# Kernel optimization log

Hardware: AMD Instinct MI355X
Metric: run time of the kernel (lower is better)

The kernel has to match this reference:

```python
import jax, jax.numpy as jnp
import numpy as np

def setup_inputs() -> dict:
    key = jax.random.key(0)
    k0, k1, k2, k3 = jax.random.split(key, 4)
    B, L, D, E, Dg = 2, 2048, 2048, 8, 256  # Dg = D // E
    x = jax.random.normal(k0, (B, L, D), dtype=jnp.float32)
    Wg = jax.random.normal(k1, (E, D), dtype=jnp.float32) * 0.02     # gate: Linear(D, E)
    Wd = jax.random.normal(k2, (E, Dg, D), dtype=jnp.float32) * 0.02  # down: Linear(D, Dg) per expert
    Wu = jax.random.normal(k3, (E, D, Dg), dtype=jnp.float32) * 0.02  # up:   Linear(Dg, D) per expert
    return {"x": x, "Wg": Wg, "Wd": Wd, "Wu": Wu, "k": 2}

def reference(x, Wg, Wd, Wu, k):
    B, L, D = x.shape
    E = Wg.shape[0]
    T = B * L
    xf = x.reshape(T, D)
    # gate scores: sigmoid(x @ Wg^T), then top-k gate values G and expert indices I
    S = jax.nn.sigmoid(xf @ Wg.T)            # [T, E]
    G, I = jax.lax.top_k(S, k)               # [T, k], [T, k]
    # combine weights per token per expert (zero for unselected experts);
    # equivalent to the original's one_hot + per-expert gather/scatter-add.
    w = jnp.zeros((T, E), x.dtype).at[jnp.arange(T)[:, None], I].add(G)  # [T, E]
    # down: sum_e w[t,e] * (Wd[e] @ x[t])
    down = jnp.einsum('te,egd,td->tg', w, Wd, xf)   # [T, Dg]
    # inner model is identity
    # up: sum_e w[t,e] * (Wu[e] @ down[t])
    up = jnp.einsum('te,edg,tg->td', w, Wu, down)   # [T, D]
    return up.reshape(B, L, D)
```

## Files before the change

kernel.cpp:

```cpp
#include <hip/hip_runtime.h>
#include <stdint.h>

#define T_TOK 4096
#define DIM   2048
#define NEXP  8
#define DG    256
#define TOPK  2

#define BM 64
#define BN 128
#define BKU 64
#define NROWS  (T_TOK*TOPK + NEXP*BM)
#define NBLK_M (NROWS/BM)

typedef __attribute__((ext_vector_type(8))) short short8;
typedef __attribute__((ext_vector_type(4))) float f32x4;

static __device__ __forceinline__ short f2bf(float f) {
    union { float f; uint32_t u; } v{f};
    uint32_t r = v.u + 0x7fffu + ((v.u >> 16) & 1u);
    return (short)(r >> 16);
}
static __device__ __forceinline__ float b2f(short s) {
    union { uint32_t u; float f; } v{((uint32_t)(unsigned short)s) << 16};
    return v.f;
}

#define GLD16(g, l) \
    __builtin_amdgcn_global_load_lds((const __attribute__((address_space(1))) void*)(g), \
                                     (__attribute__((address_space(3))) void*)(l), 16, 0, 0)

__global__ __launch_bounds__(256) void gate_kernel(const float* __restrict__ x,
                                                   const float* __restrict__ Wg,
                                                   int* __restrict__ gidx,
                                                   float* __restrict__ gval,
                                                   short* __restrict__ x_bf)
{
    int token = blockIdx.x * 4 + (threadIdx.x >> 6);
    int lane  = threadIdx.x & 63;
    const float4* xr = (const float4*)(x + (size_t)token * DIM);

    float4 xv[8];
#pragma unroll
    for (int i = 0; i < 8; i++) xv[i] = xr[lane + 64 * i];

    short4* xb = (short4*)(x_bf + (size_t)token * DIM);
#pragma unroll
    for (int i = 0; i < 8; i++) {
        short4 o;
        o.x = f2bf(xv[i].x); o.y = f2bf(xv[i].y);
        o.z = f2bf(xv[i].z); o.w = f2bf(xv[i].w);
        xb[lane + 64 * i] = o;
    }

    float acc[NEXP];
#pragma unroll
    for (int e = 0; e < NEXP; e++) {
        const float4* wr = (const float4*)(Wg + e * DIM);
        float a = 0.0f;
#pragma unroll
        for (int i = 0; i < 8; i++) {
            float4 w = wr[lane + 64 * i];
            a += xv[i].x * w.x + xv[i].y * w.y + xv[i].z * w.z + xv[i].w * w.w;
        }
        acc[e] = a;
    }

#pragma unroll
    for (int m = 1; m < 64; m <<= 1) {
#pragma unroll
        for (int e = 0; e < NEXP; e++) acc[e] += __shfl_xor(acc[e], m, 64);
    }

    if (lane == 0) {
        float sg[NEXP];
#pragma unroll
        for (int e = 0; e < NEXP; e++) sg[e] = 1.0f / (1.0f + expf(-acc[e]));
        int i0 = 0;
#pragma unroll
        for (int e = 1; e < NEXP; e++) if (sg[e] > sg[i0]) i0 = e;
        int i1 = (i0 == 0) ? 1 : 0;
#pragma unroll
        for (int e = 0; e < NEXP; e++) if (e != i0 && e != i1 && sg[e] > sg[i1]) i1 = e;
        gidx[2 * token + 0] = i0;
        gidx[2 * token + 1] = i1;
        gval[2 * token + 0] = sg[i0];
        gval[2 * token + 1] = sg[i1];
    }
}

__global__ __launch_bounds__(256) void convW_kernel(const float* __restrict__ Wd,
                                                    const float* __restrict__ Wu,
                                                    short* __restrict__ Wd_bf,
                                                    short* __restrict__ Wu_bf,
                                                    int n4)
{
    int i = blockIdx.x * 256 + threadIdx.x;
    const float* s; short* d; int j;
    if (i < n4)      { s = Wd; d = Wd_bf; j = i; }
    else             { s = Wu; d = Wu_bf; j = i - n4; if (j >= n4) return; }
    float4 v = ((const float4*)s)[j];
    short4 o;
    o.x = f2bf(v.x); o.y = f2bf(v.y); o.z = f2bf(v.z); o.w = f2bf(v.w);
    ((short4*)d)[j] = o;
}

__global__ __launch_bounds__(1024) void bucket_kernel(const int* __restrict__ gidx,
                                                      int* __restrict__ rowtok,
                                                      int* __restrict__ rowpos,
                                                      int* __restrict__ seg_off)
{
    __shared__ int cnt[NEXP];
    __shared__ int cur[NEXP];
    int tid = threadIdx.x, lane = tid & 63;
    if (tid < NEXP) cnt[tid] = 0;
    __syncthreads();

    int e_[8];
#pragma unroll
    for (int r = 0; r < 8; r++) e_[r] = gidx[r * 1024 + tid];

    int mycnt = 0;
#pragma unroll
    for (int r = 0; r < 8; r++) {
        int e = e_[r];
#pragma unroll
        for (int ee = 0; ee < NEXP; ee++) {
            unsigned long long m = __ballot(e == ee);
            if (lane == ee) mycnt += (int)__popcll(m);
        }
    }
    if (lane < NEXP) atomicAdd(&cnt[lane], mycnt);
    __syncthreads();

    if (tid == 0) {
        int o = 0;
        for (int e = 0; e < NEXP; e++) {
            seg_off[e] = o;
            cur[e] = o;
            o += ((cnt[e] + BM - 1) / BM) * BM;
        }
        seg_off[NEXP] = o;
    }
    __syncthreads();

    for (int r = tid; r < NROWS; r += 1024) rowtok[r] = -1;
    __syncthreads();

#pragma unroll
    for (int r = 0; r < 8; r++) {
        int idx = r * 1024 + tid;
        int e = e_[r];
#pragma unroll
        for (int ee = 0; ee < NEXP; ee++) {
            unsigned long long m = __ballot(e == ee);
            if (m == 0) continue;
            int leader = __ffsll((unsigned long long)m) - 1;
            int base = 0;
            if (lane == leader) base = atomicAdd(&cur[ee], (int)__popcll(m));
            base = __shfl(base, leader, 64);
            if (e == ee) {
                int pos = base + (int)__popcll(m & ((1ull << lane) - 1ull));
                rowtok[pos] = idx >> 1;
                rowpos[idx] = pos;
            }
        }
    }
}

#define AS3 __attribute__((address_space(3)))

#define VMCNT(N) asm volatile("s_waitcnt vmcnt(" #N ")" ::: "memory")
#define BAR()    __builtin_amdgcn_s_barrier()

#define STAGE(B_) do { \
    GLD16(agA0, lA_##B_##_0); \
    GLD16(agA1, lA_##B_##_1); \
    GLD16(agB0, lB_##B_##_0); \
    GLD16(agB1, lB_##B_##_1); \
    GLD16(agB2, lB_##B_##_2); \
    GLD16(agB3, lB_##B_##_3); \
    agA0 += BKU; agA1 += BKU; \
    agB0 += BKU; agB1 += BKU; agB2 += BKU; agB3 += BKU; \
} while (0)

#define COMP(B_) do { \
    short8 a00 = *(const short8*)&As[B_][am0][c0]; \
    short8 a10 = *(const short8*)&As[B_][am1][c0]; \
    short8 b00 = *(const short8*)&Bs[B_][bn0][c0]; \
    short8 b10 = *(const short8*)&Bs[B_][bn1][c0]; \
    short8 b20 = *(const short8*)&Bs[B_][bn2][c0]; \
    short8 b30 = *(const short8*)&Bs[B_][bn3][c0]; \
    short8 a01 = *(const short8*)&As[B_][am0][c1]; \
    short8 a11 = *(const short8*)&As[B_][am1][c1]; \
    short8 b01 = *(const short8*)&Bs[B_][bn0][c1]; \
    short8 b11 = *(const short8*)&Bs[B_][bn1][c1]; \
    short8 b21 = *(const short8*)&Bs[B_][bn2][c1]; \
    short8 b31 = *(const short8*)&Bs[B_][bn3][c1]; \
    acc[0][0] = __builtin_amdgcn_mfma_f32_16x16x32_bf16(a00, b00, acc[0][0], 0, 0, 0); \
    acc[0][1] = __builtin_amdgcn_mfma_f32_16x16x32_bf16(a00, b10, acc[0][1], 0, 0, 0); \
    acc[0][2] = __builtin_amdgcn_mfma_f32_16x16x32_bf16(a00, b20, acc[0][2], 0, 0, 0); \
    acc[0][3] = __builtin_amdgcn_mfma_f32_16x16x32_bf16(a00, b30, acc[0][3], 0, 0, 0); \
    acc[1][0] = __builtin_amdgcn_mfma_f32_16x16x32_bf16(a10, b00, acc[1][0], 0, 0, 0); \
    acc[1][1] = __builtin_amdgcn_mfma_f32_16x16x32_bf16(a10, b10, acc[1][1], 0, 0, 0); \
    acc[1][2] = __builtin_amdgcn_mfma_f32_16x16x32_bf16(a10, b20, acc[1][2], 0, 0, 0); \
    acc[1][3] = __builtin_amdgcn_mfma_f32_16x16x32_bf16(a10, b30, acc[1][3], 0, 0, 0); \
    acc[0][0] = __builtin_amdgcn_mfma_f32_16x16x32_bf16(a01, b01, acc[0][0], 0, 0, 0); \
    acc[0][1] = __builtin_amdgcn_mfma_f32_16x16x32_bf16(a01, b11, acc[0][1], 0, 0, 0); \
    acc[0][2] = __builtin_amdgcn_mfma_f32_16x16x32_bf16(a01, b21, acc[0][2], 0, 0, 0); \
    acc[0][3] = __builtin_amdgcn_mfma_f32_16x16x32_bf16(a01, b31, acc[0][3], 0, 0, 0); \
    acc[1][0] = __builtin_amdgcn_mfma_f32_16x16x32_bf16(a11, b01, acc[1][0], 0, 0, 0); \
    acc[1][1] = __builtin_amdgcn_mfma_f32_16x16x32_bf16(a11, b11, acc[1][1], 0, 0, 0); \
    acc[1][2] = __builtin_amdgcn_mfma_f32_16x16x32_bf16(a11, b21, acc[1][2], 0, 0, 0); \
    acc[1][3] = __builtin_amdgcn_mfma_f32_16x16x32_bf16(a11, b31, acc[1][3], 0, 0, 0); \
} while (0)

template<int K, int Ntot>
__global__ __launch_bounds__(256) void gemm_kernel(const short* __restrict__ A,
                                                   const short* __restrict__ B,
                                                   const int* __restrict__ rowtok,
                                                   const int* __restrict__ seg_off,
                                                   short* __restrict__ C)
{
    __shared__ __align__(16) short As[2][BM][BKU];
    __shared__ __align__(16) short Bs[2][BN][BKU];

    int row0 = blockIdx.x * BM;
    int total = seg_off[NEXP];
    if (row0 >= total) return;
    int e = 0;
    while (row0 >= seg_off[e + 1]) ++e;
    int n0 = blockIdx.y * BN;

    int tid = threadIdx.x;
    int w = tid >> 6, l = tid & 63;

    int srow = (w << 3) + (l >> 3);
    int sc   = ((l & 7) ^ ((l >> 3) & 7)) << 3;

    int ta0 = rowtok[row0 + srow];      if (ta0 < 0) ta0 = 0;
    int ta1 = rowtok[row0 + 32 + srow]; if (ta1 < 0) ta1 = 0;
    const short* agA0 = A + (size_t)ta0 * K + sc;
    const short* agA1 = A + (size_t)ta1 * K + sc;
    const short* be = B + (size_t)e * Ntot * K + (size_t)n0 * K;
    const short* agB0 = be + (size_t)(srow     ) * K + sc;
    const short* agB1 = be + (size_t)(srow + 32) * K + sc;
    const short* agB2 = be + (size_t)(srow + 64) * K + sc;
    const short* agB3 = be + (size_t)(srow + 96) * K + sc;

    auto lA_0_0 = (AS3 void*)&As[0][(w << 3)     ][0];
    auto lA_0_1 = (AS3 void*)&As[0][(w << 3) + 32][0];
    auto lA_1_0 = (AS3 void*)&As[1][(w << 3)     ][0];
    auto lA_1_1 = (AS3 void*)&As[1][(w << 3) + 32][0];
    auto lB_0_0 = (AS3 void*)&Bs[0][(w << 3)     ][0];
    auto lB_0_1 = (AS3 void*)&Bs[0][(w << 3) + 32][0];
    auto lB_0_2 = (AS3 void*)&Bs[0][(w << 3) + 64][0];
    auto lB_0_3 = (AS3 void*)&Bs[0][(w << 3) + 96][0];
    auto lB_1_0 = (AS3 void*)&Bs[1][(w << 3)     ][0];
    auto lB_1_1 = (AS3 void*)&Bs[1][(w << 3) + 32][0];
    auto lB_1_2 = (AS3 void*)&Bs[1][(w << 3) + 64][0];
    auto lB_1_3 = (AS3 void*)&Bs[1][(w << 3) + 96][0];

    int mlane = l & 15, qlane = l >> 4;
    int wm = w >> 1, wn = w & 1;
    int c0 = (qlane ^ (mlane & 7)) << 3;
    int c1 = c0 ^ 32;
    int am0 = wm * 32 + mlane, am1 = am0 + 16;
    int bn0 = wn * 64 + mlane, bn1 = bn0 + 16, bn2 = bn0 + 32, bn3 = bn0 + 48;

    f32x4 acc[2][4] = {};

    constexpr int NT = K / BKU;
    STAGE(0);
    STAGE(1);
#pragma unroll 1
    for (int t = 0; t < NT - 2; t += 2) {
        VMCNT(6); BAR();
        COMP(0);
        BAR();
        STAGE(0);
        VMCNT(6); BAR();
        COMP(1);
        BAR();
        if (t + 3 < NT) STAGE(1);
    }
    VMCNT(6); BAR();
    COMP(0);
    BAR();
    VMCNT(0); BAR();
    COMP(1);

#pragma unroll
    for (int i = 0; i < 2; i++) {
        int rbase = row0 + wm * 32 + i * 16 + qlane * 4;
#pragma unroll
        for (int j = 0; j < 4; j++) {
            int col = n0 + wn * 64 + j * 16 + mlane;
#pragma unroll
            for (int r = 0; r < 4; r++)
                C[(size_t)(rbase + r) * Ntot + col] = f2bf(acc[i][j][r]);
        }
    }
}

#undef STAGE
#undef COMP
#undef AS3

__global__ __launch_bounds__(256) void combine1_kernel(const short* __restrict__ dr,
                                                       const int* __restrict__ rowpos,
                                                       const float* __restrict__ gval,
                                                       short* __restrict__ dt)
{
    int t = blockIdx.x, d = threadIdx.x;
    int   p0 = rowpos[2 * t], p1 = rowpos[2 * t + 1];
    float g0 = gval[2 * t],   g1 = gval[2 * t + 1];
    float v = g0 * b2f(dr[(size_t)p0 * DG + d]) + g1 * b2f(dr[(size_t)p1 * DG + d]);
    dt[(size_t)t * DG + d] = f2bf(v);
}

__global__ __launch_bounds__(256) void combine2_kernel(const short* __restrict__ ur,
                                                       const int* __restrict__ rowpos,
                                                       const float* __restrict__ gval,
                                                       float* __restrict__ out)
{
    int i = blockIdx.x * 256 + threadIdx.x;
    int t = i >> 9;
    int c = (i & 511) * 4;
    int   p0 = rowpos[2 * t], p1 = rowpos[2 * t + 1];
    float g0 = gval[2 * t],   g1 = gval[2 * t + 1];
    short4 u0 = *(const short4*)&ur[(size_t)p0 * DIM + c];
    short4 u1 = *(const short4*)&ur[(size_t)p1 * DIM + c];
    float4 o;
    o.x = g0 * b2f(u0.x) + g1 * b2f(u1.x);
    o.y = g0 * b2f(u0.y) + g1 * b2f(u1.y);
    o.z = g0 * b2f(u0.z) + g1 * b2f(u1.z);
    o.w = g0 * b2f(u0.w) + g1 * b2f(u1.w);
    *(float4*)&out[(size_t)t * DIM + c] = o;
}

extern "C" void kernel_launch(void* const* d_in, const int* in_sizes, int n_in,
                              void* d_out, int out_size, void* d_ws, size_t ws_size,
                              hipStream_t stream) {
    const float* x  = (const float*)d_in[0];
    const float* Wg = (const float*)d_in[1];
    const float* Wd = (const float*)d_in[2];
    const float* Wu = (const float*)d_in[3];
    float* out = (float*)d_out;

    char* p = (char*)d_ws;
    int*   gidx    = (int*)(p + 0);
    float* gval    = (float*)(p + 32768);
    int*   rowtok  = (int*)(p + 65536);
    int*   rowpos  = (int*)(p + 100352);
    int*   seg_off = (int*)(p + 133120);
    short* x_bf    = (short*)(p + 133376);
    short* Wd_bf   = (short*)(p + 133376 + 16777216);
    short* Wu_bf   = Wd_bf + 4194304;
    short* dr_bf   = Wu_bf + 4194304;
    short* dt_bf   = dr_bf + (size_t)NROWS * DG;
    short* ur_bf   = dt_bf + (size_t)T_TOK * DG;

    const int W4 = NEXP * DG * DIM / 4;
    gate_kernel<<<T_TOK / 4, 256, 0, stream>>>(x, Wg, gidx, gval, x_bf);
    convW_kernel<<<(2 * W4 + 255) / 256, 256, 0, stream>>>(Wd, Wu, Wd_bf, Wu_bf, W4);
    bucket_kernel<<<1, 1024, 0, stream>>>(gidx, rowtok, rowpos, seg_off);

    gemm_kernel<DIM, DG><<<dim3(NBLK_M, DG / BN), 256, 0, stream>>>(x_bf, Wd_bf, rowtok, seg_off, dr_bf);
    combine1_kernel<<<T_TOK, 256, 0, stream>>>(dr_bf, rowpos, gval, dt_bf);
    gemm_kernel<DG, DIM><<<dim3(NBLK_M, DIM / BN), 256, 0, stream>>>(dt_bf, Wu_bf, rowtok, seg_off, ur_bf);
    combine2_kernel<<<T_TOK * DIM / 4 / 256, 256, 0, stream>>>(ur_bf, rowpos, gval, out);
}
```

Before: 204.9 us.

## Fuse gate with weight conversion, fold combine1 into up-GEMM, remap blocks for XCDs

```diff
diff --git a/kernel.cpp b/kernel.cpp
--- a/kernel.cpp
+++ b/kernel.cpp
@@ -30,12 +30,29 @@
     __builtin_amdgcn_global_load_lds((const __attribute__((address_space(1))) void*)(g), \
                                      (__attribute__((address_space(3))) void*)(l), 16, 0, 0)
 
-__global__ __launch_bounds__(256) void gate_kernel(const float* __restrict__ x,
-                                                   const float* __restrict__ Wg,
-                                                   int* __restrict__ gidx,
-                                                   float* __restrict__ gval,
-                                                   short* __restrict__ x_bf)
+__global__ __launch_bounds__(256) void gateconv_kernel(const float* __restrict__ x,
+                                                       const float* __restrict__ Wg,
+                                                       const float* __restrict__ Wd,
+                                                       const float* __restrict__ Wu,
+                                                       int* __restrict__ gidx,
+                                                       float* __restrict__ gval,
+                                                       short* __restrict__ x_bf,
+                                                       short* __restrict__ Wd_bf,
+                                                       short* __restrict__ Wu_bf)
 {
+    if (blockIdx.x >= 1024) {
+        const int n4 = NEXP * DG * DIM / 4;
+        int i = (blockIdx.x - 1024) * 256 + threadIdx.x;
+        const float* s; short* d; int j;
+        if (i < n4) { s = Wd; d = Wd_bf; j = i; }
+        else        { s = Wu; d = Wu_bf; j = i - n4; }
+        float4 v = ((const float4*)s)[j];
+        short4 o;
+        o.x = f2bf(v.x); o.y = f2bf(v.y); o.z = f2bf(v.z); o.w = f2bf(v.w);
+        ((short4*)d)[j] = o;
+        return;
+    }
+
     int token = blockIdx.x * 4 + (threadIdx.x >> 6);
     int lane  = threadIdx.x & 63;
     const float4* xr = (const float4*)(x + (size_t)token * DIM);
@@ -87,22 +104,6 @@
         gval[2 * token + 0] = sg[i0];
         gval[2 * token + 1] = sg[i1];
     }
-}
-
-__global__ __launch_bounds__(256) void convW_kernel(const float* __restrict__ Wd,
-                                                    const float* __restrict__ Wu,
-                                                    short* __restrict__ Wd_bf,
-                                                    short* __restrict__ Wu_bf,
-                                                    int n4)
-{
-    int i = blockIdx.x * 256 + threadIdx.x;
-    const float* s; short* d; int j;
-    if (i < n4)      { s = Wd; d = Wd_bf; j = i; }
-    else             { s = Wu; d = Wu_bf; j = i - n4; if (j >= n4) return; }
-    float4 v = ((const float4*)s)[j];
-    short4 o;
-    o.x = f2bf(v.x); o.y = f2bf(v.y); o.z = f2bf(v.z); o.w = f2bf(v.w);
-    ((short4*)d)[j] = o;
 }
 
 __global__ __launch_bounds__(1024) void bucket_kernel(const int* __restrict__ gidx,
@@ -215,22 +216,26 @@
     acc[1][3] = __builtin_amdgcn_mfma_f32_16x16x32_bf16(a11, b31, acc[1][3], 0, 0, 0); \
 } while (0)
 
-template<int K, int Ntot>
-__global__ __launch_bounds__(256) void gemm_kernel(const short* __restrict__ A,
-                                                   const short* __restrict__ B,
-                                                   const int* __restrict__ rowtok,
-                                                   const int* __restrict__ seg_off,
-                                                   short* __restrict__ C)
+__global__ __launch_bounds__(256) void gemm_down_kernel(const short* __restrict__ A,
+                                                        const short* __restrict__ B,
+                                                        const int* __restrict__ rowtok,
+                                                        const int* __restrict__ seg_off,
+                                                        short* __restrict__ C)
 {
+    constexpr int K = DIM, Ntot = DG;
     __shared__ __align__(16) short As[2][BM][BKU];
     __shared__ __align__(16) short Bs[2][BN][BKU];
 
-    int row0 = blockIdx.x * BM;
+    int d = blockIdx.x;
+    int lid = (d & 7) * 34 + (d >> 3);
+    int bx = lid >> 1, by = lid & 1;
+
+    int row0 = bx * BM;
     int total = seg_off[NEXP];
     if (row0 >= total) return;
     int e = 0;
     while (row0 >= seg_off[e + 1]) ++e;
-    int n0 = blockIdx.y * BN;
+    int n0 = by * BN;
 
     int tid = threadIdx.x;
     int w = tid >> 6, l = tid & 63;
@@ -304,20 +309,126 @@
 }
 
 #undef STAGE
+
+#define STAGE_B(B_) do { \
+    GLD16(agB0, lB_##B_##_0); \
+    GLD16(agB1, lB_##B_##_1); \
+    GLD16(agB2, lB_##B_##_2); \
+    GLD16(agB3, lB_##B_##_3); \
+    agB0 += BKU; agB1 += BKU; agB2 += BKU; agB3 += BKU; \
+} while (0)
+
+#define STAGE_A(B_, kb) do { \
+    short8 v0 = *(const short8*)(dr00 + (kb)); \
+    short8 v1 = *(const short8*)(dr01 + (kb)); \
+    short8 u0 = *(const short8*)(dr10 + (kb)); \
+    short8 u1 = *(const short8*)(dr11 + (kb)); \
+    short8 o0, o1; \
+    _Pragma("unroll") \
+    for (int j = 0; j < 8; j++) { \
+        o0[j] = f2bf(g00 * b2f(v0[j]) + g01 * b2f(v1[j])); \
+        o1[j] = f2bf(g10 * b2f(u0[j]) + g11 * b2f(u1[j])); \
+    } \
+    *(short8*)&As[B_][srow     ][cl] = o0; \
+    *(short8*)&As[B_][srow + 32][cl] = o1; \
+} while (0)
+
+__global__ __launch_bounds__(256) void gemm_up_kernel(const short* __restrict__ dr,
+                                                      const short* __restrict__ B,
+                                                      const int* __restrict__ rowtok,
+                                                      const int* __restrict__ rowpos,
+                                                      const float* __restrict__ gval,
+                                                      const int* __restrict__ seg_off,
+                                                      short* __restrict__ C)
+{
+    constexpr int K = DG, Ntot = DIM;
+    __shared__ __align__(16) short As[2][BM][BKU];
+    __shared__ __align__(16) short Bs[2][BN][BKU];
+
+    int d = blockIdx.x;
+    int lid = (d & 7) * 272 + (d >> 3);
+    int bx = lid % NBLK_M;
+    int by = lid / NBLK_M;
+
+    int row0 = bx * BM;
+    int total = seg_off[NEXP];
+    if (row0 >= total) return;
+    int e = 0;
+    while (row0 >= seg_off[e + 1]) ++e;
+    int n0 = by * BN;
+
+    int tid = threadIdx.x;
+    int w = tid >> 6, l = tid & 63;
+
+    int srow = (w << 3) + (l >> 3);
+    int sc   = ((l & 7) ^ ((l >> 3) & 7)) << 3;
+    int cl   = (l & 7) << 3;
+
+    int t0 = rowtok[row0 + srow];      if (t0 < 0) t0 = 0;
+    int t1 = rowtok[row0 + 32 + srow]; if (t1 < 0) t1 = 0;
+    int   p00 = rowpos[2 * t0], p01 = rowpos[2 * t0 + 1];
+    int   p10 = rowpos[2 * t1], p11 = rowpos[2 * t1 + 1];
+    float g00 = gval[2 * t0],   g01 = gval[2 * t0 + 1];
+    float g10 = gval[2 * t1],   g11 = gval[2 * t1 + 1];
+    const short* dr00 = dr + (size_t)p00 * DG + sc;
+    const short* dr01 = dr + (size_t)p01 * DG + sc;
+    const short* dr10 = dr + (size_t)p10 * DG + sc;
+    const short* dr11 = dr + (size_t)p11 * DG + sc;
+
+    const short* be = B + (size_t)e * Ntot * K + (size_t)n0 * K;
+    const short* agB0 = be + (size_t)(srow     ) * K + sc;
+    const short* agB1 = be + (size_t)(srow + 32) * K + sc;
+    const short* agB2 = be + (size_t)(srow + 64) * K + sc;
+    const short* agB3 = be + (size_t)(srow + 96) * K + sc;
+
+    auto lB_0_0 = (AS3 void*)&Bs[0][(w << 3)     ][0];
+    auto lB_0_1 = (AS3 void*)&Bs[0][(w << 3) + 32][0];
+    auto lB_0_2 = (AS3 void*)&Bs[0][(w << 3) + 64][0];
+    auto lB_0_3 = (AS3 void*)&Bs[0][(w << 3) + 96][0];
+    auto lB_1_0 = (AS3 void*)&Bs[1][(w << 3)     ][0];
+    auto lB_1_1 = (AS3 void*)&Bs[1][(w << 3) + 32][0];
+    auto lB_1_2 = (AS3 void*)&Bs[1][(w << 3) + 64][0];
+    auto lB_1_3 = (AS3 void*)&Bs[1][(w << 3) + 96][0];
+
+    int mlane = l & 15, qlane = l >> 4;
+    int wm = w >> 1, wn = w & 1;
+    int c0 = (qlane ^ (mlane & 7)) << 3;
+    int c1 = c0 ^ 32;
+    int am0 = wm * 32 + mlane, am1 = am0 + 16;
+    int bn0 = wn * 64 + mlane, bn1 = bn0 + 16, bn2 = bn0 + 32, bn3 = bn0 + 48;
+
+    f32x4 acc[2][4] = {};
+
+    STAGE_A(0, 0); STAGE_B(0);
+    __syncthreads();
+    STAGE_A(1, BKU); STAGE_B(1);
+    COMP(0);
+    __syncthreads();
+    STAGE_A(0, 2 * BKU); STAGE_B(0);
+    COMP(1);
+    __syncthreads();
+    STAGE_A(1, 3 * BKU); STAGE_B(1);
+    COMP(0);
+    __syncthreads();
+    COMP(1);
+
+#pragma unroll
+    for (int i = 0; i < 2; i++) {
+        int rbase = row0 + wm * 32 + i * 16 + qlane * 4;
+#pragma unroll
+        for (int j = 0; j < 4; j++) {
+            int col = n0 + wn * 64 + j * 16 + mlane;
+#pragma unroll
+            for (int r = 0; r < 4; r++)
+                C[(size_t)(rbase + r) * Ntot + col] = f2bf(acc[i][j][r]);
+        }
+    }
+}
+
+#undef STAGE_A
+#undef STAGE_B
 #undef COMP
 #undef AS3
-
-__global__ __launch_bounds__(256) void combine1_kernel(const short* __restrict__ dr,
-                                                       const int* __restrict__ rowpos,
-                                                       const float* __restrict__ gval,
-                                                       short* __restrict__ dt)
-{
-    int t = blockIdx.x, d = threadIdx.x;
-    int   p0 = rowpos[2 * t], p1 = rowpos[2 * t + 1];
-    float g0 = gval[2 * t],   g1 = gval[2 * t + 1];
-    float v = g0 * b2f(dr[(size_t)p0 * DG + d]) + g1 * b2f(dr[(size_t)p1 * DG + d]);
-    dt[(size_t)t * DG + d] = f2bf(v);
-}
 
 __global__ __launch_bounds__(256) void combine2_kernel(const short* __restrict__ ur,
                                                        const int* __restrict__ rowpos,
@@ -358,16 +469,11 @@
     short* Wd_bf   = (short*)(p + 133376 + 16777216);
     short* Wu_bf   = Wd_bf + 4194304;
     short* dr_bf   = Wu_bf + 4194304;
-    short* dt_bf   = dr_bf + (size_t)NROWS * DG;
-    short* ur_bf   = dt_bf + (size_t)T_TOK * DG;
-
-    const int W4 = NEXP * DG * DIM / 4;
-    gate_kernel<<<T_TOK / 4, 256, 0, stream>>>(x, Wg, gidx, gval, x_bf);
-    convW_kernel<<<(2 * W4 + 255) / 256, 256, 0, stream>>>(Wd, Wu, Wd_bf, Wu_bf, W4);
+    short* ur_bf   = dr_bf + (size_t)NROWS * DG;
+
+    gateconv_kernel<<<9216, 256, 0, stream>>>(x, Wg, Wd, Wu, gidx, gval, x_bf, Wd_bf, Wu_bf);
     bucket_kernel<<<1, 1024, 0, stream>>>(gidx, rowtok, rowpos, seg_off);
-
-    gemm_kernel<DIM, DG><<<dim3(NBLK_M, DG / BN), 256, 0, stream>>>(x_bf, Wd_bf, rowtok, seg_off, dr_bf);
-    combine1_kernel<<<T_TOK, 256, 0, stream>>>(dr_bf, rowpos, gval, dt_bf);
-    gemm_kernel<DG, DIM><<<dim3(NBLK_M, DIM / BN), 256, 0, stream>>>(dt_bf, Wu_bf, rowtok, seg_off, ur_bf);
+    gemm_down_kernel<<<NBLK_M * (DG / BN), 256, 0, stream>>>(x_bf, Wd_bf, rowtok, seg_off, dr_bf);
+    gemm_up_kernel<<<NBLK_M * (DIM / BN), 256, 0, stream>>>(dr_bf, Wu_bf, rowtok, rowpos, gval, seg_off, ur_bf);
     combine2_kernel<<<T_TOK * DIM / 4 / 256, 256, 0, stream>>>(ur_bf, rowpos, gval, out);
 }
```

After: 204.0 us. No clear change (-0.4%).
